# Kernel optimization log

Hardware: AMD Instinct MI355X
Metric: run time of the kernel (lower is better)

## Reference

```python
import jax, jax.numpy as jnp
import numpy as np

B, L, WIN = 65536, 240, 24
EMB_SZS = [(367, 20), (7, 4), (24, 8)]
N_CONT = 16
H1, H2, OUT_SZ = 512, 256, 24
N_EMB = sum(nf for _, nf in EMB_SZS)
NUM_WAVE = 6 * (WIN // 2) + 6 * (WIN // 4)  # 108


def pool_matrix(lin, w):
    # PyTorch AdaptiveAvgPool1d: bin i averages x[floor(i*lin/w) : ceil((i+1)*lin/w)]
    P = np.zeros((lin, w), np.float32)
    for i in range(w):
        s = (i * lin) // w
        e = -((-(i + 1) * lin) // w)
        P[s:e, i] = 1.0 / (e - s)
    return jnp.asarray(P)


def conv1(x, w, dil):
    # single-channel 1D cross-correlation, no bias; x: [B, Lin], w: [ks]
    ks = w.shape[0]
    lout = x.shape[-1] - dil * (ks - 1)
    return sum(w[k] * x[:, k * dil:k * dil + lout] for k in range(ks))


def branch(xw, wa, wb):
    # conv(ks, dil=1) -> adaptive_avg_pool(12) -> leaky_relu(0.1), then same with dil=2 -> pool(6)
    ca = conv1(xw, wa, 1)                                   # [B, L-ks+1]
    fa = jax.nn.leaky_relu(ca @ pool_matrix(ca.shape[-1], WIN // 2), 0.1)  # [B,12]
    cb = conv1(fa, wb, 2)                                   # [B, 12-2*(ks-1)]
    fb = jax.nn.leaky_relu(cb @ pool_matrix(cb.shape[-1], WIN // 4), 0.1)  # [B,6]
    return fa, fb


def setup_inputs() -> dict:
    key = jax.random.key(0)
    ks_list = list(range(1, 7))
    keys = jax.random.split(key, 32)
    d = {}
    d['x_window'] = jax.random.normal(keys[0], (B, 1, L), jnp.float32)
    cats = [jax.random.randint(jax.random.fold_in(keys[1], i), (B,), 0, ni)
            for i, (ni, _) in enumerate(EMB_SZS)]
    d['x_cat'] = jnp.stack(cats, axis=1).astype(jnp.int64)
    d['x_cont'] = jax.random.normal(keys[2], (B, N_CONT), jnp.float32)
    for i, ks in enumerate(ks_list):
        d[f'wk{ks}a'] = jax.random.normal(keys[3 + 2 * i], (ks,), jnp.float32) * 0.5
        d[f'wk{ks}b'] = jax.random.normal(keys[4 + 2 * i], (ks,), jnp.float32) * 0.5
    for i, (ni, nf) in enumerate(EMB_SZS):
        d[f'E{i}'] = jax.random.normal(keys[16 + i], (ni, nf), jnp.float32) * 0.01
    d['bn_g'] = jnp.ones((N_CONT,), jnp.float32)
    d['bn_b'] = jnp.zeros((N_CONT,), jnp.float32)
    n_in = N_EMB + N_CONT
    d['W1'] = jax.random.normal(keys[20], (n_in, H1), jnp.float32) * (1.0 / np.sqrt(n_in))
    d['b1'] = jnp.zeros((H1,), jnp.float32)
    d['W2'] = jax.random.normal(keys[21], (H1, H2), jnp.float32) * (1.0 / np.sqrt(H1))
    d['b2'] = jnp.zeros((H2,), jnp.float32)
    d['Wlin'] = jax.random.normal(keys[22], (NUM_WAVE + H2, OUT_SZ), jnp.float32) * (1.0 / np.sqrt(NUM_WAVE + H2))
    return d


def reference(x_window, x_cat, x_cont,
              wk1a, wk1b, wk2a, wk2b, wk3a, wk3b, wk4a, wk4b, wk5a, wk5b, wk6a, wk6b,
              E0, E1, E2, bn_g, bn_b, W1, b1, W2, b2, Wlin):
    xw = x_window[:, 0, :]  # [B, L]
    feats = []
    for wa, wb in [(wk1a, wk1b), (wk2a, wk2b), (wk3a, wk3b),
                   (wk4a, wk4b), (wk5a, wk5b), (wk6a, wk6b)]:
        fa, fb = branch(xw, wa, wb)
        feats += [fa, fb]
    ffc = jnp.concatenate(feats, axis=1)  # [B, 108]
    # embeddings
    emb = jnp.concatenate([E0[x_cat[:, 0]], E1[x_cat[:, 1]], E2[x_cat[:, 2]]], axis=1)  # [B, 32]
    # BatchNorm1d on continuous features (training-mode batch stats, eps=1e-5)
    m = jnp.mean(x_cont, axis=0)
    v = jnp.var(x_cont, axis=0)
    xc = (x_cont - m) / jnp.sqrt(v + 1e-5) * bn_g + bn_b
    x = jnp.concatenate([emb, xc], axis=1)  # [B, 48]
    x = jax.nn.relu(x @ W1 + b1)
    x = jax.nn.relu(x @ W2 + b2)  # [B, 256]
    fc = jnp.concatenate([ffc, x], axis=1)  # [B, 364]
    return fc @ Wlin  # [B, 24]
```

## Files before the change

kernel.cpp:

```cpp
#include <hip/hip_runtime.h>

typedef __bf16 bf16x8 __attribute__((ext_vector_type(8)));
typedef float  f32x4  __attribute__((ext_vector_type(4)));
typedef unsigned short ushort_t;

#define B_TOTAL 65536

__device__ __forceinline__ ushort_t f2bf(float f) {
  unsigned u = __builtin_bit_cast(unsigned, f);
  u += 0x7fffu + ((u >> 16) & 1u);
  return (ushort_t)(u >> 16);
}
__device__ __forceinline__ unsigned pk2(float lo, float hi) {
  unsigned r;
  asm("v_cvt_pk_bf16_f32 %0, %1, %2" : "=v"(r) : "v"(lo), "v"(hi));
  return r;
}
__device__ __forceinline__ float lrelu(float v) { return v >= 0.f ? v : 0.1f * v; }
__device__ __forceinline__ bf16x8 ld_frag(const ushort_t* p8) {
  return __builtin_bit_cast(bf16x8, *(const uint4*)p8);
}
__device__ __forceinline__ bf16x8 ld_tile(const ushort_t* base, int tile, int lane) {
  return __builtin_bit_cast(bf16x8,
      *(const uint4*)((const char*)base + tile * 1024 + lane * 16));
}
__device__ __forceinline__ char* frag_addr4(ushort_t* base, int k, int s15, int st) {
  int kb = k >> 5, g = (k >> 3) & 3, i = k & 7;
  return (char*)base + (((kb * 4 + st) * 64) + s15 + g * 16) * 16 + i * 2;
}
__device__ __forceinline__ f32x4 mfma16(bf16x8 a, bf16x8 b, f32x4 c) {
  return __builtin_amdgcn_mfma_f32_16x16x32_bf16(a, b, c, 0, 0, 0);
}

struct PrepParams {
  const float* W1; const float* W2; const float* Wl;
  ushort_t* w1p; ushort_t* w2p; ushort_t* wlp;
  ushort_t* Apack; ushort_t* Bpack;
  const float* xc; float* ws;
  const float* wk[12];
};

__global__ __launch_bounds__(256) void prep_all(PrepParams q) {
  __shared__ float red[512];
  const int b = blockIdx.x, t = threadIdx.x;
  if (b < 688) {
    int u = b * 256 + t;
    if (u < 32768) {
      int i = u & 7, lane = (u >> 3) & 63, kb = u >> 14;
      int k = kb * 32 + ((lane >> 4) << 3) + i;
      int n = (((u >> 9) & 31) << 4) + (lane & 15);
      q.w1p[u] = f2bf(k < 48 ? q.W1[k * 512 + n] : 0.f);
    } else if (u < 32768 + 131072) {
      int v = u - 32768;
      int i = v & 7, lane = (v >> 3) & 63, kb = v >> 13;
      int k = kb * 32 + ((lane >> 4) << 3) + i;
      int n = (((v >> 9) & 15) << 4) + (lane & 15);
      q.w2p[v] = f2bf(q.W2[k * 256 + n]);
    } else {
      int v = u - (32768 + 131072);
      int i = v & 7, lane = (v >> 3) & 63, kb = v >> 10;
      int k = kb * 32 + ((lane >> 4) << 3) + i;
      int n = (((v >> 9) & 1) << 4) + (lane & 15);
      float val = 0.f;
      if (n < 24) {
        if (k < 108)       val = q.Wl[k * 24 + n];
        else if (k >= 128) val = q.Wl[(k - 20) * 24 + n];
      }
      q.wlp[v] = f2bf(val);
    }
  } else if (b < 792) {
    int u = (b - 688) * 256 + t;
    if (u < 20480) {
      int i = u & 7, lane = (u >> 3) & 63;
      int knt = u >> 9;
      int kb = knt / 5, nt = knt % 5;
      int k = kb * 32 + ((lane >> 4) << 3) + i;
      int n = nt * 16 + (lane & 15);
      float val = 0.f;
      if (n < 72 && k < 240) {
        int br = n / 12, ii = n - br * 12, ks = br + 1, lin = 240 - br;
        int si = ii * lin / 12, ei = ((ii + 1) * lin + 11) / 12;
        const float* wa = q.wk[2 * br];
        float acc = 0.f;
        for (int kk = 0; kk < ks; ++kk) {
          int j = k - kk;
          if (j >= si && j < ei) acc += wa[kk];
        }
        val = acc / (float)(ei - si);
      }
      q.Apack[u] = f2bf(val);
    } else {
      int v = u - 20480;
      int i = v & 7, lane = (v >> 3) & 63;
      int knt = v >> 9;
      int kb = knt / 3, nt = knt % 3;
      int kcol = kb * 32 + ((lane >> 4) << 3) + i;
      int n = nt * 16 + (lane & 15);
      float val = 0.f;
      if (n < 36 && kcol < 108) {
        int brk = kcol / 18, ii = kcol - brk * 18;
        int brn = n / 6, j = n - brn * 6;
        if (brk == brn && ii < 12) {
          int ks = brn + 1, lcb = 12 - 2 * brn;
          int sj = j * lcb / 6, ej = ((j + 1) * lcb + 5) / 6;
          const float* wb = q.wk[2 * brn + 1];
          float acc = 0.f;
          for (int kk = 0; kk < ks; ++kk) {
            int qq = ii - 2 * kk;
            if (qq >= sj && qq < ej) acc += wb[kk];
          }
          val = acc / (float)(ej - sj);
        }
      }
      q.Bpack[v] = f2bf(val);
    }
  } else {
    const int c = t & 15, g = t >> 4;
    const int r0 = (b - 792) * 256;
    float s = 0.f, qq = 0.f;
    for (int i = 0; i < 16; ++i) {
      float v = q.xc[(size_t)(r0 + g + i * 16) * 16 + c];
      s += v; qq += v * v;
    }
    red[t] = s; red[256 + t] = qq;
    __syncthreads();
    if (t < 16) {
      float ss = 0.f, sq = 0.f;
      for (int gg = 0; gg < 16; ++gg) { ss += red[gg * 16 + t]; sq += red[256 + gg * 16 + t]; }
      q.ws[(b - 792) * 32 + t] = ss;
      q.ws[(b - 792) * 32 + 16 + t] = sq;
    }
  }
}

struct FusedParams {
  const float* xw;
  const int*   xcat;
  const float* xcont;
  const float* E0; const float* E1; const float* E2;
  const float* b1; const float* b2;
  const ushort_t* Apack; const ushort_t* Bpack;
  const ushort_t* w1p; const ushort_t* w2p; const ushort_t* wlp;
  const float* bnws;
  const float* bn_g; const float* bn_b;
  float*       out;
};

__global__ __launch_bounds__(1024, 8) void fused_kernel(FusedParams p) {
  __shared__ __align__(16) char smem[57472];
  ushort_t* s_xw  = (ushort_t*)smem;
  ushort_t* s_h1  = (ushort_t*)smem;
  ushort_t* s_h2  = (ushort_t*)smem;
  ushort_t* s_cf  = (ushort_t*)(smem + 32768);
  ushort_t* s_x48 = (ushort_t*)(smem + 49152);
  float*    s_bn  = (float*)(smem + 57344);

  const int t    = threadIdx.x;
  const int lane = t & 63;
  const int w    = t >> 6;
  const int quad = lane >> 4;
  const int s15  = lane & 15;
  const int s0   = blockIdx.x * 64;
  const f32x4 fzero = {0.f, 0.f, 0.f, 0.f};

  for (int u = t; u < 64 * 60; u += 1024) {
    int s = u / 60, m4 = u - s * 60;
    float4 v = *(const float4*)(p.xw + (size_t)(s0 + s) * 240 + 4 * m4);
    uint2 pkv; pkv.x = pk2(v.x, v.y); pkv.y = pk2(v.z, v.w);
    int tile = (m4 >> 3) * 4 + (s >> 4);
    *(uint2*)((char*)s_xw + (tile * 64 + (s & 15) + ((m4 >> 1) & 3) * 16) * 16
              + (m4 & 1) * 8) = pkv;
  }
  float* redbuf = (float*)s_x48;
  if (t < 512) {
    int c = t & 31, g16 = t >> 5;
    float acc = 0.f;
    for (int i = 0; i < 16; ++i) acc += p.bnws[(g16 * 16 + i) * 32 + c];
    redbuf[g16 * 32 + c] = acc;
  }
  ((uint4*)s_cf)[t] = uint4{0, 0, 0, 0};
  if (t >= 512 && t < 640) {
    int tt = t - 512;
    *(uint4*)((char*)s_xw + (28 + (tt >> 5)) * 1024 + 512 + (tt & 31) * 16) = uint4{0, 0, 0, 0};
  }
  __syncthreads();
  if (t < 16) {
    float ss = 0.f, sq = 0.f;
    for (int g = 0; g < 16; ++g) { ss += redbuf[g * 32 + t]; sq += redbuf[g * 32 + 16 + t]; }
    float mean  = ss / (float)B_TOTAL;
    float var   = sq / (float)B_TOTAL - mean * mean;
    float scale = p.bn_g[t] / sqrtf(var + 1e-5f);
    s_bn[t]      = scale;
    s_bn[16 + t] = p.bn_b[t] - mean * scale;
  }
  __syncthreads();
  if (t < 128) {
    *(uint4*)((char*)s_x48 + (4 + (t >> 5)) * 1024 + 512 + (t & 31) * 16) = uint4{0, 0, 0, 0};
  }
  for (int u = t; u < 64 * 48; u += 1024) {
    int s = u / 48, c = u - s * 48, gs = s0 + s;
    float v;
    if (c < 20)      v = p.E0[(size_t)p.xcat[gs * 3 + 0] * 20 + c];
    else if (c < 24) v = p.E1[(size_t)p.xcat[gs * 3 + 1] * 4 + (c - 20)];
    else if (c < 32) v = p.E2[(size_t)p.xcat[gs * 3 + 2] * 8 + (c - 24)];
    else { int cc = c - 32; v = p.xcont[(size_t)gs * 16 + cc] * s_bn[cc] + s_bn[16 + cc]; }
    *(ushort_t*)frag_addr4(s_x48, c, s & 15, s >> 4) = f2bf(v);
  }
  __syncthreads();

  auto do0a = [&](int nt, int st) {
    f32x4 acc = fzero;
    #pragma unroll
    for (int kb = 0; kb < 8; ++kb) {
      bf16x8 a = ld_frag(p.Apack + (size_t)((kb * 5 + nt) * 64 + lane) * 8);
      bf16x8 b = ld_tile(s_xw, kb * 4 + st, lane);
      acc = mfma16(a, b, acc);
    }
    int n0 = nt * 16 + quad * 4;
    int br = n0 / 12;
    int col0 = n0 + 6 * br;
    *(unsigned*)frag_addr4(s_cf, col0, s15, st)     = pk2(lrelu(acc[0]), lrelu(acc[1]));
    *(unsigned*)frag_addr4(s_cf, col0 + 2, s15, st) = pk2(lrelu(acc[2]), lrelu(acc[3]));
  };
  do0a(w % 5, w / 5);
  if (w < 4) do0a((w + 16) % 5, (w + 16) / 5);
  __syncthreads();

  const int np = w >> 1;
  const int sh = w & 1;

  const int ntB = w % 3, stB = w / 3;
  f32x4 accB = fzero;
  if (w < 12) {
    #pragma unroll
    for (int kb = 0; kb < 4; ++kb) {
      bf16x8 a = ld_frag(p.Bpack + (size_t)((kb * 3 + ntB) * 64 + lane) * 8);
      bf16x8 b = ld_tile(s_cf, kb * 4 + stB, lane);
      accB = mfma16(a, b, accB);
    }
  }

  auto gemm1_half = [&](int h) {
    int gnt = h * 16 + w;
    bf16x8 a0 = ld_frag(p.w1p + (size_t)((0 * 32 + gnt) * 64 + lane) * 8);
    bf16x8 a1 = ld_frag(p.w1p + (size_t)((32 + gnt) * 64 + lane) * 8);
    int n0l = w * 16 + quad * 4;
    float4 bb = *(const float4*)(p.b1 + h * 256 + n0l);
    int kb1 = w >> 1;
    int g   = (w * 2 + (quad >> 1)) & 3;
    #pragma unroll
    for (int st = 0; st < 4; ++st) {
      bf16x8 b0 = ld_tile(s_x48, st, lane);
      bf16x8 b1 = ld_tile(s_x48, 4 + st, lane);
      f32x4 acc = mfma16(a0, b0, fzero);
      acc = mfma16(a1, b1, acc);
      float v0 = fmaxf(acc[0] + bb.x, 0.f);
      float v1 = fmaxf(acc[1] + bb.y, 0.f);
      float v2 = fmaxf(acc[2] + bb.z, 0.f);
      float v3 = fmaxf(acc[3] + bb.w, 0.f);
      uint2 pkv; pkv.x = pk2(v0, v1); pkv.y = pk2(v2, v3);
      *(uint2*)((char*)s_h1 + ((kb1 * 4 + st) * 64 + s15 + g * 16) * 16
                + (quad & 1) * 8) = pkv;
    }
  };
  gemm1_half(0);

  uint4 pa[2][2];
  pa[0][0] = *(const uint4*)(p.w2p + (size_t)((0 * 16 + 2 * np + 0) * 64 + lane) * 8);
  pa[0][1] = *(const uint4*)(p.w2p + (size_t)((0 * 16 + 2 * np + 1) * 64 + lane) * 8);
  pa[1][0] = *(const uint4*)(p.w2p + (size_t)((1 * 16 + 2 * np + 0) * 64 + lane) * 8);
  pa[1][1] = *(const uint4*)(p.w2p + (size_t)((1 * 16 + 2 * np + 1) * 64 + lane) * 8);
  __syncthreads();

  if (w < 12) {
    int n0 = ntB * 16 + quad * 4;
    if (n0 < 36) {
      int br0 = n0 / 6, c0 = n0 + 12 * (br0 + 1);
      int n2 = n0 + 2, br2 = n2 / 6, c2 = n2 + 12 * (br2 + 1);
      *(unsigned*)frag_addr4(s_cf, c0, s15, stB) = pk2(lrelu(accB[0]), lrelu(accB[1]));
      *(unsigned*)frag_addr4(s_cf, c2, s15, stB) = pk2(lrelu(accB[2]), lrelu(accB[3]));
    }
  }

  f32x4 acc2[2][2];
  #pragma unroll
  for (int jm = 0; jm < 2; ++jm) { acc2[jm][0] = fzero; acc2[jm][1] = fzero; }

  auto gemm2_half = [&](int k0) {
    #pragma unroll
    for (int kk = 0; kk < 8; ++kk) {
      int kb = k0 + kk;
      bf16x8 a0 = __builtin_bit_cast(bf16x8, pa[kb & 1][0]);
      bf16x8 a1 = __builtin_bit_cast(bf16x8, pa[kb & 1][1]);
      if (kk < 6) {
        pa[kb & 1][0] = *(const uint4*)(p.w2p + (size_t)(((kb + 2) * 16 + 2 * np + 0) * 64 + lane) * 8);
        pa[kb & 1][1] = *(const uint4*)(p.w2p + (size_t)(((kb + 2) * 16 + 2 * np + 1) * 64 + lane) * 8);
      }
      #pragma unroll
      for (int sl = 0; sl < 2; ++sl) {
        bf16x8 b = ld_tile(s_h1, kk * 4 + 2 * sh + sl, lane);
        acc2[0][sl] = mfma16(a0, b, acc2[0][sl]);
        acc2[1][sl] = mfma16(a1, b, acc2[1][sl]);
      }
    }
  };
  gemm2_half(0);
  __syncthreads();

  gemm1_half(1);
  pa[0][0] = *(const uint4*)(p.w2p + (size_t)((8 * 16 + 2 * np + 0) * 64 + lane) * 8);
  pa[0][1] = *(const uint4*)(p.w2p + (size_t)((8 * 16 + 2 * np + 1) * 64 + lane) * 8);
  pa[1][0] = *(const uint4*)(p.w2p + (size_t)((9 * 16 + 2 * np + 0) * 64 + lane) * 8);
  pa[1][1] = *(const uint4*)(p.w2p + (size_t)((9 * 16 + 2 * np + 1) * 64 + lane) * 8);
  __syncthreads();

  gemm2_half(8);
  __syncthreads();

  #pragma unroll
  for (int jm = 0; jm < 2; ++jm) {
    int nt = 2 * np + jm;
    int n0 = nt * 16 + quad * 4;
    float4 bb = *(const float4*)(p.b2 + n0);
    int kbh = nt >> 1;
    int g   = (nt * 2 + (quad >> 1)) & 3;
    #pragma unroll
    for (int sl = 0; sl < 2; ++sl) {
      int st = 2 * sh + sl;
      float v0 = fmaxf(acc2[jm][sl][0] + bb.x, 0.f);
      float v1 = fmaxf(acc2[jm][sl][1] + bb.y, 0.f);
      float v2 = fmaxf(acc2[jm][sl][2] + bb.z, 0.f);
      float v3 = fmaxf(acc2[jm][sl][3] + bb.w, 0.f);
      uint2 pkv; pkv.x = pk2(v0, v1); pkv.y = pk2(v2, v3);
      *(uint2*)((char*)s_h2 + ((kbh * 4 + st) * 64 + s15 + g * 16) * 16
                + (quad & 1) * 8) = pkv;
    }
  }
  __syncthreads();

  if (w < 8) {
    const int st = w & 3, nt = w >> 2;
    f32x4 acc = fzero;
    #pragma unroll
    for (int kb = 0; kb < 12; ++kb) {
      bf16x8 a = ld_frag(p.wlp + (size_t)((kb * 2 + nt) * 64 + lane) * 8);
      bf16x8 b = (kb < 4) ? ld_tile(s_cf, kb * 4 + st, lane)
                          : ld_tile(s_h2, (kb - 4) * 4 + st, lane);
      acc = mfma16(a, b, acc);
    }
    int n0 = nt * 16 + quad * 4;
    if (n0 < 24) {
      int sg = s0 + st * 16 + s15;
      *(float2*)(p.out + (size_t)sg * 24 + n0)     = make_float2(acc[0], acc[1]);
      *(float2*)(p.out + (size_t)sg * 24 + n0 + 2) = make_float2(acc[2], acc[3]);
    }
  }
}

extern "C" void kernel_launch(void* const* d_in, const int* in_sizes, int n_in,
                              void* d_out, int out_size, void* d_ws, size_t ws_size,
                              hipStream_t stream) {
  const float* xcont = (const float*)d_in[2];
  float* ws  = (float*)d_ws;
  char*  wsb = (char*)d_ws;
  ushort_t* w1p   = (ushort_t*)(wsb + 36864);
  ushort_t* w2p   = (ushort_t*)(wsb + 102400);
  ushort_t* wlp   = (ushort_t*)(wsb + 364544);
  ushort_t* Apack = (ushort_t*)(wsb + 389120);
  ushort_t* Bpack = (ushort_t*)(wsb + 430080);

  PrepParams q;
  q.W1 = (const float*)d_in[20]; q.W2 = (const float*)d_in[22]; q.Wl = (const float*)d_in[24];
  q.w1p = w1p; q.w2p = w2p; q.wlp = wlp;
  q.Apack = Apack; q.Bpack = Bpack;
  q.xc = xcont; q.ws = ws;
  for (int i = 0; i < 12; ++i) q.wk[i] = (const float*)d_in[3 + i];
  prep_all<<<1048, 256, 0, stream>>>(q);

  FusedParams p;
  p.xw    = (const float*)d_in[0];
  p.xcat  = (const int*)d_in[1];
  p.xcont = xcont;
  p.E0 = (const float*)d_in[15]; p.E1 = (const float*)d_in[16]; p.E2 = (const float*)d_in[17];
  p.b1 = (const float*)d_in[21]; p.b2 = (const float*)d_in[23];
  p.Apack = Apack; p.Bpack = Bpack;
  p.w1p = w1p; p.w2p = w2p; p.wlp = wlp;
  p.bnws = ws;
  p.bn_g = (const float*)d_in[18]; p.bn_b = (const float*)d_in[19];
  p.out = (float*)d_out;
  fused_kernel<<<B_TOTAL / 64, 1024, 0, stream>>>(p);
}
```

Before: 61.28 us.

## Split BN finalize into own kernel and pipeline GEMM1/GEMM2 in quarter chunks

Batch-norm statistics are now reduced once in a separate single-block kernel that writes scale and shift to the workspace, instead of every fused block re-reducing 256x32 partials plus two extra barriers. The hidden-layer GEMMs are restructured into four quarter chunks with double-buffered shared memory, so GEMM1 for chunk q+1 overlaps GEMM2 for chunk q, and each wave now owns one GEMM2 output tile across all 4 sample tiles. This adds a kernel launch and changes the per-wave W2 fragment prefetch pattern and the number of barriers.

```diff
diff --git a/kernel.cpp b/kernel.cpp
--- a/kernel.cpp
+++ b/kernel.cpp
@@ -133,6 +133,32 @@
   }
 }
 
+__global__ __launch_bounds__(256) void bn_final(const float* __restrict__ ws_in,
+                                                float* __restrict__ ws_out,
+                                                const float* __restrict__ g_,
+                                                const float* __restrict__ b_) {
+  __shared__ float red[512];
+  const int t = threadIdx.x;
+  const int c = t & 15, g = t >> 4;
+  float s = 0.f, q = 0.f;
+  for (int i = 0; i < 16; ++i) {
+    int blk = g * 16 + i;
+    s += ws_in[blk * 32 + c];
+    q += ws_in[blk * 32 + 16 + c];
+  }
+  red[t] = s; red[256 + t] = q;
+  __syncthreads();
+  if (t < 16) {
+    float ss = 0.f, qq = 0.f;
+    for (int gg = 0; gg < 16; ++gg) { ss += red[gg * 16 + t]; qq += red[256 + gg * 16 + t]; }
+    float mean  = ss / (float)B_TOTAL;
+    float var   = qq / (float)B_TOTAL - mean * mean;
+    float scale = g_[t] / sqrtf(var + 1e-5f);
+    ws_out[8192 + t]      = scale;
+    ws_out[8192 + 16 + t] = b_[t] - mean * scale;
+  }
+}
+
 struct FusedParams {
   const float* xw;
   const int*   xcat;
@@ -141,19 +167,18 @@
   const float* b1; const float* b2;
   const ushort_t* Apack; const ushort_t* Bpack;
   const ushort_t* w1p; const ushort_t* w2p; const ushort_t* wlp;
-  const float* bnws;
-  const float* bn_g; const float* bn_b;
+  const float* stats;
   float*       out;
 };
 
 __global__ __launch_bounds__(1024, 8) void fused_kernel(FusedParams p) {
-  __shared__ __align__(16) char smem[57472];
+  __shared__ __align__(16) char smem[57344];
   ushort_t* s_xw  = (ushort_t*)smem;
-  ushort_t* s_h1  = (ushort_t*)smem;
   ushort_t* s_h2  = (ushort_t*)smem;
+  ushort_t* qbuf0 = (ushort_t*)smem;
+  ushort_t* qbuf1 = (ushort_t*)(smem + 16384);
   ushort_t* s_cf  = (ushort_t*)(smem + 32768);
   ushort_t* s_x48 = (ushort_t*)(smem + 49152);
-  float*    s_bn  = (float*)(smem + 57344);
 
   const int t    = threadIdx.x;
   const int lane = t & 63;
@@ -163,6 +188,13 @@
   const int s0   = blockIdx.x * 64;
   const f32x4 fzero = {0.f, 0.f, 0.f, 0.f};
 
+  ((uint4*)s_cf)[t] = uint4{0, 0, 0, 0};
+  if (t < 128) {
+    *(uint4*)((char*)s_xw + (28 + (t >> 5)) * 1024 + 512 + (t & 31) * 16) = uint4{0, 0, 0, 0};
+  } else if (t < 256) {
+    int tt = t - 128;
+    *(uint4*)((char*)s_x48 + (4 + (tt >> 5)) * 1024 + 512 + (tt & 31) * 16) = uint4{0, 0, 0, 0};
+  }
   for (int u = t; u < 64 * 60; u += 1024) {
     int s = u / 60, m4 = u - s * 60;
     float4 v = *(const float4*)(p.xw + (size_t)(s0 + s) * 240 + 4 * m4);
@@ -171,39 +203,13 @@
     *(uint2*)((char*)s_xw + (tile * 64 + (s & 15) + ((m4 >> 1) & 3) * 16) * 16
               + (m4 & 1) * 8) = pkv;
   }
-  float* redbuf = (float*)s_x48;
-  if (t < 512) {
-    int c = t & 31, g16 = t >> 5;
-    float acc = 0.f;
-    for (int i = 0; i < 16; ++i) acc += p.bnws[(g16 * 16 + i) * 32 + c];
-    redbuf[g16 * 32 + c] = acc;
-  }
-  ((uint4*)s_cf)[t] = uint4{0, 0, 0, 0};
-  if (t >= 512 && t < 640) {
-    int tt = t - 512;
-    *(uint4*)((char*)s_xw + (28 + (tt >> 5)) * 1024 + 512 + (tt & 31) * 16) = uint4{0, 0, 0, 0};
-  }
-  __syncthreads();
-  if (t < 16) {
-    float ss = 0.f, sq = 0.f;
-    for (int g = 0; g < 16; ++g) { ss += redbuf[g * 32 + t]; sq += redbuf[g * 32 + 16 + t]; }
-    float mean  = ss / (float)B_TOTAL;
-    float var   = sq / (float)B_TOTAL - mean * mean;
-    float scale = p.bn_g[t] / sqrtf(var + 1e-5f);
-    s_bn[t]      = scale;
-    s_bn[16 + t] = p.bn_b[t] - mean * scale;
-  }
-  __syncthreads();
-  if (t < 128) {
-    *(uint4*)((char*)s_x48 + (4 + (t >> 5)) * 1024 + 512 + (t & 31) * 16) = uint4{0, 0, 0, 0};
-  }
   for (int u = t; u < 64 * 48; u += 1024) {
     int s = u / 48, c = u - s * 48, gs = s0 + s;
     float v;
     if (c < 20)      v = p.E0[(size_t)p.xcat[gs * 3 + 0] * 20 + c];
     else if (c < 24) v = p.E1[(size_t)p.xcat[gs * 3 + 1] * 4 + (c - 20)];
     else if (c < 32) v = p.E2[(size_t)p.xcat[gs * 3 + 2] * 8 + (c - 24)];
-    else { int cc = c - 32; v = p.xcont[(size_t)gs * 16 + cc] * s_bn[cc] + s_bn[16 + cc]; }
+    else { int cc = c - 32; v = p.xcont[(size_t)gs * 16 + cc] * p.stats[cc] + p.stats[16 + cc]; }
     *(ushort_t*)frag_addr4(s_x48, c, s & 15, s >> 4) = f2bf(v);
   }
   __syncthreads();
@@ -224,32 +230,25 @@
   };
   do0a(w % 5, w / 5);
   if (w < 4) do0a((w + 16) % 5, (w + 16) / 5);
-  __syncthreads();
-
-  const int np = w >> 1;
-  const int sh = w & 1;
-
-  const int ntB = w % 3, stB = w / 3;
-  f32x4 accB = fzero;
-  if (w < 12) {
-    #pragma unroll
-    for (int kb = 0; kb < 4; ++kb) {
-      bf16x8 a = ld_frag(p.Bpack + (size_t)((kb * 3 + ntB) * 64 + lane) * 8);
-      bf16x8 b = ld_tile(s_cf, kb * 4 + stB, lane);
-      accB = mfma16(a, b, accB);
-    }
-  }
-
-  auto gemm1_half = [&](int h) {
-    int gnt = h * 16 + w;
+
+  uint4 pa[2];
+  pa[0] = *(const uint4*)(p.w2p + (size_t)((0 * 16 + w) * 64 + lane) * 8);
+  pa[1] = *(const uint4*)(p.w2p + (size_t)((1 * 16 + w) * 64 + lane) * 8);
+  __syncthreads();
+
+  auto gemm1_q = [&](int q, ushort_t* qbuf) {
+    int ntl = w & 7;
+    int gnt = q * 8 + ntl;
     bf16x8 a0 = ld_frag(p.w1p + (size_t)((0 * 32 + gnt) * 64 + lane) * 8);
     bf16x8 a1 = ld_frag(p.w1p + (size_t)((32 + gnt) * 64 + lane) * 8);
-    int n0l = w * 16 + quad * 4;
-    float4 bb = *(const float4*)(p.b1 + h * 256 + n0l);
-    int kb1 = w >> 1;
-    int g   = (w * 2 + (quad >> 1)) & 3;
-    #pragma unroll
-    for (int st = 0; st < 4; ++st) {
+    int n0l = ntl * 16 + quad * 4;
+    float4 bb = *(const float4*)(p.b1 + q * 128 + n0l);
+    int kbl = ntl >> 1;
+    int g   = (ntl * 2 + (quad >> 1)) & 3;
+    int sh2 = (w >> 3) * 2;
+    #pragma unroll
+    for (int sj = 0; sj < 2; ++sj) {
+      int st = sh2 + sj;
       bf16x8 b0 = ld_tile(s_x48, st, lane);
       bf16x8 b1 = ld_tile(s_x48, 4 + st, lane);
       f32x4 acc = mfma16(a0, b0, fzero);
@@ -259,17 +258,41 @@
       float v2 = fmaxf(acc[2] + bb.z, 0.f);
       float v3 = fmaxf(acc[3] + bb.w, 0.f);
       uint2 pkv; pkv.x = pk2(v0, v1); pkv.y = pk2(v2, v3);
-      *(uint2*)((char*)s_h1 + ((kb1 * 4 + st) * 64 + s15 + g * 16) * 16
+      *(uint2*)((char*)qbuf + ((kbl * 4 + st) * 64 + s15 + g * 16) * 16
                 + (quad & 1) * 8) = pkv;
     }
   };
-  gemm1_half(0);
-
-  uint4 pa[2][2];
-  pa[0][0] = *(const uint4*)(p.w2p + (size_t)((0 * 16 + 2 * np + 0) * 64 + lane) * 8);
-  pa[0][1] = *(const uint4*)(p.w2p + (size_t)((0 * 16 + 2 * np + 1) * 64 + lane) * 8);
-  pa[1][0] = *(const uint4*)(p.w2p + (size_t)((1 * 16 + 2 * np + 0) * 64 + lane) * 8);
-  pa[1][1] = *(const uint4*)(p.w2p + (size_t)((1 * 16 + 2 * np + 1) * 64 + lane) * 8);
+
+  f32x4 acc2[4];
+  #pragma unroll
+  for (int st = 0; st < 4; ++st) acc2[st] = fzero;
+
+  auto gemm2_q = [&](int q, const ushort_t* qbuf) {
+    #pragma unroll
+    for (int kk = 0; kk < 4; ++kk) {
+      int kb = q * 4 + kk;
+      bf16x8 a0 = __builtin_bit_cast(bf16x8, pa[kb & 1]);
+      if (kb + 2 < 16)
+        pa[kb & 1] = *(const uint4*)(p.w2p + (size_t)(((kb + 2) * 16 + w) * 64 + lane) * 8);
+      #pragma unroll
+      for (int st = 0; st < 4; ++st) {
+        bf16x8 b = ld_tile(qbuf, kk * 4 + st, lane);
+        acc2[st] = mfma16(a0, b, acc2[st]);
+      }
+    }
+  };
+
+  const int ntB = w % 3, stB = w / 3;
+  f32x4 accB = fzero;
+  if (w < 12) {
+    #pragma unroll
+    for (int kb = 0; kb < 4; ++kb) {
+      bf16x8 a = ld_frag(p.Bpack + (size_t)((kb * 3 + ntB) * 64 + lane) * 8);
+      bf16x8 b = ld_tile(s_cf, kb * 4 + stB, lane);
+      accB = mfma16(a, b, accB);
+    }
+  }
+  gemm1_q(0, qbuf0);
   __syncthreads();
 
   if (w < 12) {
@@ -281,56 +304,32 @@
       *(unsigned*)frag_addr4(s_cf, c2, s15, stB) = pk2(lrelu(accB[2]), lrelu(accB[3]));
     }
   }
-
-  f32x4 acc2[2][2];
-  #pragma unroll
-  for (int jm = 0; jm < 2; ++jm) { acc2[jm][0] = fzero; acc2[jm][1] = fzero; }
-
-  auto gemm2_half = [&](int k0) {
-    #pragma unroll
-    for (int kk = 0; kk < 8; ++kk) {
-      int kb = k0 + kk;
-      bf16x8 a0 = __builtin_bit_cast(bf16x8, pa[kb & 1][0]);
-      bf16x8 a1 = __builtin_bit_cast(bf16x8, pa[kb & 1][1]);
-      if (kk < 6) {
-        pa[kb & 1][0] = *(const uint4*)(p.w2p + (size_t)(((kb + 2) * 16 + 2 * np + 0) * 64 + lane) * 8);
-        pa[kb & 1][1] = *(const uint4*)(p.w2p + (size_t)(((kb + 2) * 16 + 2 * np + 1) * 64 + lane) * 8);
-      }
-      #pragma unroll
-      for (int sl = 0; sl < 2; ++sl) {
-        bf16x8 b = ld_tile(s_h1, kk * 4 + 2 * sh + sl, lane);
-        acc2[0][sl] = mfma16(a0, b, acc2[0][sl]);
-        acc2[1][sl] = mfma16(a1, b, acc2[1][sl]);
-      }
-    }
-  };
-  gemm2_half(0);
-  __syncthreads();
-
-  gemm1_half(1);
-  pa[0][0] = *(const uint4*)(p.w2p + (size_t)((8 * 16 + 2 * np + 0) * 64 + lane) * 8);
-  pa[0][1] = *(const uint4*)(p.w2p + (size_t)((8 * 16 + 2 * np + 1) * 64 + lane) * 8);
-  pa[1][0] = *(const uint4*)(p.w2p + (size_t)((9 * 16 + 2 * np + 0) * 64 + lane) * 8);
-  pa[1][1] = *(const uint4*)(p.w2p + (size_t)((9 * 16 + 2 * np + 1) * 64 + lane) * 8);
-  __syncthreads();
-
-  gemm2_half(8);
-  __syncthreads();
-
-  #pragma unroll
-  for (int jm = 0; jm < 2; ++jm) {
-    int nt = 2 * np + jm;
-    int n0 = nt * 16 + quad * 4;
+  gemm2_q(0, qbuf0);
+  gemm1_q(1, qbuf1);
+  __syncthreads();
+
+  gemm2_q(1, qbuf1);
+  gemm1_q(2, qbuf0);
+  __syncthreads();
+
+  gemm2_q(2, qbuf0);
+  gemm1_q(3, qbuf1);
+  __syncthreads();
+
+  gemm2_q(3, qbuf1);
+  __syncthreads();
+
+  {
+    int n0 = w * 16 + quad * 4;
     float4 bb = *(const float4*)(p.b2 + n0);
-    int kbh = nt >> 1;
-    int g   = (nt * 2 + (quad >> 1)) & 3;
-    #pragma unroll
-    for (int sl = 0; sl < 2; ++sl) {
-      int st = 2 * sh + sl;
-      float v0 = fmaxf(acc2[jm][sl][0] + bb.x, 0.f);
-      float v1 = fmaxf(acc2[jm][sl][1] + bb.y, 0.f);
-      float v2 = fmaxf(acc2[jm][sl][2] + bb.z, 0.f);
-      float v3 = fmaxf(acc2[jm][sl][3] + bb.w, 0.f);
+    int kbh = w >> 1;
+    int g   = (w * 2 + (quad >> 1)) & 3;
+    #pragma unroll
+    for (int st = 0; st < 4; ++st) {
+      float v0 = fmaxf(acc2[st][0] + bb.x, 0.f);
+      float v1 = fmaxf(acc2[st][1] + bb.y, 0.f);
+      float v2 = fmaxf(acc2[st][2] + bb.z, 0.f);
+      float v3 = fmaxf(acc2[st][3] + bb.w, 0.f);
       uint2 pkv; pkv.x = pk2(v0, v1); pkv.y = pk2(v2, v3);
       *(uint2*)((char*)s_h2 + ((kbh * 4 + st) * 64 + s15 + g * 16) * 16
                 + (quad & 1) * 8) = pkv;
@@ -376,6 +375,7 @@
   q.xc = xcont; q.ws = ws;
   for (int i = 0; i < 12; ++i) q.wk[i] = (const float*)d_in[3 + i];
   prep_all<<<1048, 256, 0, stream>>>(q);
+  bn_final<<<1, 256, 0, stream>>>(ws, ws, (const float*)d_in[18], (const float*)d_in[19]);
 
   FusedParams p;
   p.xw    = (const float*)d_in[0];
@@ -385,8 +385,7 @@
   p.b1 = (const float*)d_in[21]; p.b2 = (const float*)d_in[23];
   p.Apack = Apack; p.Bpack = Bpack;
   p.w1p = w1p; p.w2p = w2p; p.wlp = wlp;
-  p.bnws = ws;
-  p.bn_g = (const float*)d_in[18]; p.bn_b = (const float*)d_in[19];
+  p.stats = ws + 8192;
   p.out = (float*)d_out;
   fused_kernel<<<B_TOTAL / 64, 1024, 0, stream>>>(p);
 }
```

Result: faster. 56.53 us, median of 3 (-7.8%).
